# Performance work log

Measured on AMD Instinct MI355X. Metric: run time of the kernel, lower is better.

Reference implementation:

```python
import jax, jax.numpy as jnp
import numpy as np

B, T, N, C = 4, 2048, 4, 1024   # batch, seq, expansion_rate, hidden_dim
A = 8                            # max_lora_adapters
SINKHORN_ITERS = 20
EPS = 1e-05


def _logit(x):
    x = jnp.clip(x, 1e-06, 1.0 - 1e-06)
    return jnp.log(x) - jnp.log(1.0 - x)


def setup_inputs() -> dict:
    key = jax.random.key(0)
    ks = jax.random.split(key, 12)
    nC = N * C
    x = jax.random.normal(ks[0], (B, T, N, C), dtype=jnp.float32)
    adapter_indices = jax.random.randint(ks[1], (B,), 0, A)
    # Learned parameters (perturbed from the identity init so gradients are non-trivial)
    input_norm_weight = 1.0 + 0.02 * jax.random.normal(ks[2], (A, nC), dtype=jnp.float32)
    phi_pre = 0.02 * jax.random.normal(ks[3], (A, nC, N), dtype=jnp.float32)
    phi_post = 0.02 * jax.random.normal(ks[4], (A, nC, N), dtype=jnp.float32)
    phi_res = 0.02 * jax.random.normal(ks[5], (A, nC, N * N), dtype=jnp.float32)
    b_pre = _logit(jnp.float32(1.0 / N)) + 0.1 * jax.random.normal(ks[6], (A, N), dtype=jnp.float32)
    b_post = 0.1 * jax.random.normal(ks[7], (A, N), dtype=jnp.float32)
    b_res = 10.0 * jnp.eye(N, dtype=jnp.float32) + jax.random.normal(ks[8], (A, N, N), dtype=jnp.float32)
    alpha_pre = 1.0 + 0.1 * jax.random.normal(ks[9], (A,), dtype=jnp.float32)
    alpha_post = 1.0 + 0.1 * jax.random.normal(ks[10], (A,), dtype=jnp.float32)
    alpha_res = 1.0 + 0.1 * jax.random.normal(ks[11], (A,), dtype=jnp.float32)
    return {
        "x": x,
        "input_norm_weight": input_norm_weight,
        "phi_pre": phi_pre, "phi_post": phi_post, "phi_res": phi_res,
        "b_pre": b_pre, "b_post": b_post, "b_res": b_res,
        "alpha_pre": alpha_pre, "alpha_post": alpha_post, "alpha_res": alpha_res,
        "adapter_indices": adapter_indices,
    }


def _sinkhorn_knopp(M, iters):
    M = jnp.exp(M)
    def step(_, mat):
        mat = mat / mat.sum(axis=-1, keepdims=True)
        mat = mat / mat.sum(axis=-2, keepdims=True)
        return mat
    return jax.lax.fori_loop(0, iters, step, M)


def reference(x, input_norm_weight, phi_pre, phi_post, phi_res,
              b_pre, b_post, b_res, alpha_pre, alpha_post, alpha_res,
              adapter_indices):
    Bb, Tt, n, Cc = x.shape
    idx = adapter_indices.astype(jnp.int32)
    x_flat = x.reshape(Bb, Tt, n * Cc)
    # adapter-indexed RMSNorm
    w = input_norm_weight[idx]                                  # [B, nC]
    rms = jnp.sqrt(jnp.mean(x_flat ** 2, axis=-1, keepdims=True) + EPS)
    x_norm = w[:, None, :] * x_flat / rms                       # [B, T, nC]
    # pre: input-dependent aggregation weights H_pre
    pre_logits = jnp.einsum('btd,bdn->btn', x_norm, phi_pre[idx])
    H_pre = jax.nn.sigmoid(alpha_pre[idx][:, None, None] * pre_logits + b_pre[idx][:, None, :])
    x_agg = (H_pre[..., None] * x).sum(axis=-2)                 # [B, T, C]
    output = x_agg                                              # identity block between pre and post
    # post: distribution weights H_post and doubly-stochastic mixing M
    post_logits = jnp.einsum('btd,bdn->btn', x_norm, phi_post[idx])
    H_post = 2.0 * jax.nn.sigmoid(alpha_post[idx][:, None, None] * post_logits + b_post[idx][:, None, :])
    res_logits = jnp.einsum('btd,bdm->btm', x_norm, phi_res[idx]).reshape(Bb, Tt, n, n)
    tilde_H_res = alpha_res[idx][:, None, None, None] * res_logits + b_res[idx][:, None, :, :]
    M = _sinkhorn_knopp(tilde_H_res, SINKHORN_ITERS)            # [B, T, n, n]
    y_dist = H_post[..., None] * output[..., None, :]           # [B, T, n, C]
    x_mixed = jnp.einsum('btij,btjc->btic', M, x)               # [B, T, n, C]
    return x_mixed + y_dist
```

## Files before the change

### kernel.cpp

```cpp
#include <hip/hip_runtime.h>


#define BT 8192
#define NC 4096
#define NC4 1024

__global__ __launch_bounds__(256, 3) void lora_connector_kernel(
    const float* __restrict__ x,
    const float* __restrict__ inw,
    const float* __restrict__ phi_pre,
    const float* __restrict__ phi_post,
    const float* __restrict__ phi_res,
    const float* __restrict__ b_pre,
    const float* __restrict__ b_post,
    const float* __restrict__ b_res,
    const float* __restrict__ alpha_pre,
    const float* __restrict__ alpha_post,
    const float* __restrict__ alpha_res,
    const int*   __restrict__ adapter_indices,
    float* __restrict__ out)
{
    const int tid = threadIdx.x;
    const int g   = tid & 3;
    const int l   = tid >> 2;
    const int wvid= tid >> 6;
    const int ln  = tid & 63;
    const int blk = blockIdx.x;
    const int b   = blk >> 9;
    const int idx = adapter_indices[b];

    const float4* __restrict__ pp4 = (const float4*)(phi_pre  + (size_t)idx * (NC * 4));
    const float4* __restrict__ po4 = (const float4*)(phi_post + (size_t)idx * (NC * 4));
    const float4* __restrict__ pr4 = (const float4*)(phi_res  + (size_t)idx * (NC * 16));
    const float*  __restrict__ inwp = inw + (size_t)idx * NC + tid;
    const float*  __restrict__ xb   = x + (size_t)(blk * 4) * NC + tid;

    __shared__ float4 tileL[2][1536];
    __shared__ float red[4][4][26];

    const float4* sg[6];
    int sstr[6];
    #pragma unroll
    for (int i = 0; i < 6; ++i) {
        const int c = wvid * 6 + i;
        const float4* bp; int off, str;
        if (c < 8) {
            bp  = (c < 4) ? pp4 : po4;
            off = ((c & 3) << 6) + ln;
            str = 256;
        } else {
            const int k = c - 8;
            bp  = pr4;
            off = ((((k & 3) << 6) + ln) << 2) + (k >> 2);
            str = 1024;
        }
        sg[i] = bp + off;
        sstr[i] = str;
    }

    #define STAGE_TILE(MT, BF)                                                   \
    {                                                                            \
        _Pragma("unroll")                                                        \
        for (int i = 0; i < 6; ++i) {                                            \
            __builtin_amdgcn_global_load_lds(                                    \
                (const __attribute__((address_space(1))) void*)(sg[i] + (size_t)(MT) * sstr[i]), \
                (__attribute__((address_space(3))) void*)&tileL[BF][(wvid * 6 + i) << 6], \
                16, 0, 0);                                                       \
        }                                                                        \
    }

    STAGE_TILE(0, 0);

    float acc[24][4];
    float ss[4];
    #pragma unroll
    for (int j = 0; j < 24; ++j) {
        acc[j][0] = 0.0f; acc[j][1] = 0.0f; acc[j][2] = 0.0f; acc[j][3] = 0.0f;
    }
    ss[0] = ss[1] = ss[2] = ss[3] = 0.0f;

    float xn[4], wn;
    #pragma unroll
    for (int j = 0; j < 4; ++j) xn[j] = xb[j * NC];
    wn = inwp[0];

    #pragma unroll 1
    for (int m = 0; m < 16; ++m) {
        const int bf = m & 1;
        __syncthreads();
        if (m < 15) STAGE_TILE(m + 1, bf ^ 1);

        const float wv = wn;
        float s[4];
        #pragma unroll
        for (int j = 0; j < 4; ++j) {
            const float xv = xn[j];
            s[j] = xv * wv;
            ss[j] = fmaf(xv, xv, ss[j]);
        }
        if (m < 15) {
            #pragma unroll
            for (int j = 0; j < 4; ++j) xn[j] = xb[j * NC + (m + 1) * 256];
            wn = inwp[(m + 1) * 256];
        }

        const float4 a = tileL[bf][tid];
        #pragma unroll
        for (int j = 0; j < 4; ++j) {
            acc[0][j] = fmaf(s[j], a.x, acc[0][j]);
            acc[1][j] = fmaf(s[j], a.y, acc[1][j]);
            acc[2][j] = fmaf(s[j], a.z, acc[2][j]);
            acc[3][j] = fmaf(s[j], a.w, acc[3][j]);
        }
        const float4 p = tileL[bf][256 + tid];
        #pragma unroll
        for (int j = 0; j < 4; ++j) {
            acc[4][j] = fmaf(s[j], p.x, acc[4][j]);
            acc[5][j] = fmaf(s[j], p.y, acc[5][j]);
            acc[6][j] = fmaf(s[j], p.z, acc[6][j]);
            acc[7][j] = fmaf(s[j], p.w, acc[7][j]);
        }
        #pragma unroll
        for (int q = 0; q < 4; ++q) {
            const float4 r = tileL[bf][512 + q * 256 + tid];
            #pragma unroll
            for (int j = 0; j < 4; ++j) {
                acc[8 + q * 4 + 0][j] = fmaf(s[j], r.x, acc[8 + q * 4 + 0][j]);
                acc[8 + q * 4 + 1][j] = fmaf(s[j], r.y, acc[8 + q * 4 + 1][j]);
                acc[8 + q * 4 + 2][j] = fmaf(s[j], r.z, acc[8 + q * 4 + 2][j]);
                acc[8 + q * 4 + 3][j] = fmaf(s[j], r.w, acc[8 + q * 4 + 3][j]);
            }
        }
    }

    float tot[25];
    #define RED4(V0, V1, V2, V3, DST)                                   \
    {                                                                   \
        const float u0 = (V0) + __shfl_xor((V0), 1);                    \
        const float u1 = (V1) + __shfl_xor((V1), 1);                    \
        const float u2 = (V2) + __shfl_xor((V2), 1);                    \
        const float u3 = (V3) + __shfl_xor((V3), 1);                    \
        const float r0 = (ln & 1) ? u1 : u0;                            \
        const float r1 = (ln & 1) ? u3 : u2;                            \
        const float w0 = r0 + __shfl_xor(r0, 2);                        \
        const float w1 = r1 + __shfl_xor(r1, 2);                        \
        float tv = (ln & 2) ? w1 : w0;                                  \
        tv += __shfl_xor(tv, 4);  tv += __shfl_xor(tv, 8);              \
        tv += __shfl_xor(tv, 16); tv += __shfl_xor(tv, 32);             \
        (DST) = tv;                                                     \
    }
    #pragma unroll
    for (int j = 0; j < 24; ++j)
        RED4(acc[j][0], acc[j][1], acc[j][2], acc[j][3], tot[j]);
    RED4(ss[0], ss[1], ss[2], ss[3], tot[24]);
    #undef RED4

    if (ln < 4) {
        #pragma unroll
        for (int j = 0; j < 25; ++j) red[wvid][ln][j] = tot[j];
    }
    __syncthreads();
    #pragma unroll
    for (int j = 0; j < 25; ++j)
        tot[j] = (red[0][g][j] + red[1][g][j]) + (red[2][g][j] + red[3][g][j]);

    const float inv_rms = rsqrtf(tot[24] * (1.0f / 4096.0f) + 1e-5f);
    const float apre  = alpha_pre[idx];
    const float apost = alpha_post[idx];
    const float ares  = alpha_res[idx];

    float Hpre[4], Hpost[4];
    #pragma unroll
    for (int n = 0; n < 4; ++n) {
        const float zp = fmaf(apre,  tot[n]     * inv_rms, b_pre[idx * 4 + n]);
        Hpre[n]  = 1.0f / (1.0f + __expf(-zp));
        const float zq = fmaf(apost, tot[4 + n] * inv_rms, b_post[idx * 4 + n]);
        Hpost[n] = 2.0f / (1.0f + __expf(-zq));
    }

    const int s16 = ln >> 2;
    const int sj = s16 & 3;
    const int si = s16 >> 2;
    float Mv = __expf(fmaf(ares, tot[8 + si * 4 + sj] * inv_rms,
                           b_res[idx * 16 + si * 4 + sj]));
    #pragma unroll
    for (int it = 0; it < 20; ++it) {
        float rs = Mv + __shfl_xor(Mv, 4);
        rs += __shfl_xor(rs, 8);
        Mv *= __builtin_amdgcn_rcpf(rs);
        float cs = Mv + __shfl_xor(Mv, 16);
        cs += __shfl_xor(cs, 32);
        Mv *= __builtin_amdgcn_rcpf(cs);
    }

    float W[4][4];
    #pragma unroll
    for (int sq = 0; sq < 16; ++sq) {
        const float mm = __shfl(Mv, sq * 4 + g);
        W[sq >> 2][sq & 3] = fmaf(Hpost[sq >> 2], Hpre[sq & 3], mm);
    }

    const int tok = blk * 4 + g;
    const float4* __restrict__ x4p = (const float4*)x + (size_t)tok * NC4;
    float4* __restrict__ out4 = (float4*)out + (size_t)tok * NC4;
    #pragma unroll
    for (int k = 0; k < 4; ++k) {
        const int c4 = k * 64 + l;
        const float4 x0 = x4p[0 * 256 + c4];
        const float4 x1 = x4p[1 * 256 + c4];
        const float4 x2 = x4p[2 * 256 + c4];
        const float4 x3 = x4p[3 * 256 + c4];
        #pragma unroll
        for (int i = 0; i < 4; ++i) {
            float4 o;
            o.x = fmaf(W[i][0], x0.x, fmaf(W[i][1], x1.x, fmaf(W[i][2], x2.x, W[i][3] * x3.x)));
            o.y = fmaf(W[i][0], x0.y, fmaf(W[i][1], x1.y, fmaf(W[i][2], x2.y, W[i][3] * x3.y)));
            o.z = fmaf(W[i][0], x0.z, fmaf(W[i][1], x1.z, fmaf(W[i][2], x2.z, W[i][3] * x3.z)));
            o.w = fmaf(W[i][0], x0.w, fmaf(W[i][1], x1.w, fmaf(W[i][2], x2.w, W[i][3] * x3.w)));
            out4[i * 256 + c4] = o;
        }
    }
    #undef STAGE_TILE
}

extern "C" void kernel_launch(void* const* d_in, const int* in_sizes, int n_in,
                              void* d_out, int out_size, void* d_ws, size_t ws_size,
                              hipStream_t stream) {
    const float* x         = (const float*)d_in[0];
    const float* inw       = (const float*)d_in[1];
    const float* phi_pre   = (const float*)d_in[2];
    const float* phi_post  = (const float*)d_in[3];
    const float* phi_res   = (const float*)d_in[4];
    const float* b_pre     = (const float*)d_in[5];
    const float* b_post    = (const float*)d_in[6];
    const float* b_res     = (const float*)d_in[7];
    const float* alpha_pre = (const float*)d_in[8];
    const float* alpha_post= (const float*)d_in[9];
    const float* alpha_res = (const float*)d_in[10];
    const int*   adapter   = (const int*)d_in[11];
    float* out = (float*)d_out;

    dim3 grid(BT / 4);
    dim3 block(256);
    lora_connector_kernel<<<grid, block, 0, stream>>>(
        x, inw, phi_pre, phi_post, phi_res,
        b_pre, b_post, b_res,
        alpha_pre, alpha_post, alpha_res,
        adapter, out);
}
```

Before: 333.0 us.

## Split projection outputs across block halves to halve accumulator registers

Each half of the 256-thread block now accumulates 12 of the 24 projection outputs over 128-element d-tiles, with twice as many tiles (32 instead of 16). The half-size LDS double buffer and the 48 accumulators per thread instead of 96 aim to relieve register pressure and raise occupancy, which is why the minimum-blocks launch bound is dropped. In exchange, both halves load the same x and norm-weight values, there are more loop iterations and barriers, and the cross-wave reduction is remapped. The LDS destination address passed to global_load_lds now includes a per-lane offset, which may not match how that builtin addresses LDS.

```diff
diff --git a/kernel.cpp b/kernel.cpp
--- a/kernel.cpp
+++ b/kernel.cpp
@@ -4,8 +4,10 @@
 #define BT 8192
 #define NC 4096
 #define NC4 1024
-
-__global__ __launch_bounds__(256, 3) void lora_connector_kernel(
+#define NT 32
+#define TD 128
+
+__global__ __launch_bounds__(256) void lora_connector_kernel(
     const float* __restrict__ x,
     const float* __restrict__ inw,
     const float* __restrict__ phi_pre,
@@ -25,6 +27,8 @@
     const int l   = tid >> 2;
     const int wvid= tid >> 6;
     const int ln  = tid & 63;
+    const int dl  = tid & 127;
+    const int half= tid >> 7;
     const int blk = blockIdx.x;
     const int b   = blk >> 9;
     const int idx = adapter_indices[b];
@@ -32,27 +36,27 @@
     const float4* __restrict__ pp4 = (const float4*)(phi_pre  + (size_t)idx * (NC * 4));
     const float4* __restrict__ po4 = (const float4*)(phi_post + (size_t)idx * (NC * 4));
     const float4* __restrict__ pr4 = (const float4*)(phi_res  + (size_t)idx * (NC * 16));
-    const float*  __restrict__ inwp = inw + (size_t)idx * NC + tid;
-    const float*  __restrict__ xb   = x + (size_t)(blk * 4) * NC + tid;
-
-    __shared__ float4 tileL[2][1536];
-    __shared__ float red[4][4][26];
-
-    const float4* sg[6];
-    int sstr[6];
-    #pragma unroll
-    for (int i = 0; i < 6; ++i) {
-        const int c = wvid * 6 + i;
+    const float*  __restrict__ inwp = inw + (size_t)idx * NC + dl;
+    const float*  __restrict__ xb   = x + (size_t)(blk * 4) * NC + dl;
+
+    __shared__ float4 tileL[2][768];
+    __shared__ float red[4][4][14];
+
+    const float4* sg[3];
+    int sstr[3];
+    #pragma unroll
+    for (int i = 0; i < 3; ++i) {
+        const int c = wvid * 3 + i;
         const float4* bp; int off, str;
-        if (c < 8) {
-            bp  = (c < 4) ? pp4 : po4;
-            off = ((c & 3) << 6) + ln;
-            str = 256;
+        if (c < 4) {
+            bp  = (c < 2) ? pp4 : po4;
+            off = ((c & 1) << 6) + ln;
+            str = TD;
         } else {
-            const int k = c - 8;
+            const int k = c - 4;
             bp  = pr4;
-            off = ((((k & 3) << 6) + ln) << 2) + (k >> 2);
-            str = 1024;
+            off = ((((k & 1) << 6) + ln) << 2) + (k >> 1);
+            str = TD * 4;
         }
         sg[i] = bp + off;
         sstr[i] = str;
@@ -61,20 +65,20 @@
     #define STAGE_TILE(MT, BF)                                                   \
     {                                                                            \
         _Pragma("unroll")                                                        \
-        for (int i = 0; i < 6; ++i) {                                            \
+        for (int i = 0; i < 3; ++i) {                                            \
             __builtin_amdgcn_global_load_lds(                                    \
                 (const __attribute__((address_space(1))) void*)(sg[i] + (size_t)(MT) * sstr[i]), \
-                (__attribute__((address_space(3))) void*)&tileL[BF][(wvid * 6 + i) << 6], \
+                (__attribute__((address_space(3))) void*)&tileL[BF][((wvid * 3 + i) << 6) + ln], \
                 16, 0, 0);                                                       \
         }                                                                        \
     }
 
     STAGE_TILE(0, 0);
 
-    float acc[24][4];
+    float acc[12][4];
     float ss[4];
     #pragma unroll
-    for (int j = 0; j < 24; ++j) {
+    for (int j = 0; j < 12; ++j) {
         acc[j][0] = 0.0f; acc[j][1] = 0.0f; acc[j][2] = 0.0f; acc[j][3] = 0.0f;
     }
     ss[0] = ss[1] = ss[2] = ss[3] = 0.0f;
@@ -84,11 +88,13 @@
     for (int j = 0; j < 4; ++j) xn[j] = xb[j * NC];
     wn = inwp[0];
 
+    const int ba = half * 384 + dl;
+
     #pragma unroll 1
-    for (int m = 0; m < 16; ++m) {
+    for (int m = 0; m < NT; ++m) {
         const int bf = m & 1;
         __syncthreads();
-        if (m < 15) STAGE_TILE(m + 1, bf ^ 1);
+        if (m < NT - 1) STAGE_TILE(m + 1, bf ^ 1);
 
         const float wv = wn;
         float s[4];
@@ -98,42 +104,33 @@
             s[j] = xv * wv;
             ss[j] = fmaf(xv, xv, ss[j]);
         }
-        if (m < 15) {
+        if (m < NT - 1) {
             #pragma unroll
-            for (int j = 0; j < 4; ++j) xn[j] = xb[j * NC + (m + 1) * 256];
-            wn = inwp[(m + 1) * 256];
-        }
-
-        const float4 a = tileL[bf][tid];
+            for (int j = 0; j < 4; ++j) xn[j] = xb[j * NC + (m + 1) * TD];
+            wn = inwp[(m + 1) * TD];
+        }
+
+        const float4 a = tileL[bf][ba];
+        const float4 p = tileL[bf][ba + 128];
+        const float4 r = tileL[bf][ba + 256];
         #pragma unroll
         for (int j = 0; j < 4; ++j) {
-            acc[0][j] = fmaf(s[j], a.x, acc[0][j]);
-            acc[1][j] = fmaf(s[j], a.y, acc[1][j]);
-            acc[2][j] = fmaf(s[j], a.z, acc[2][j]);
-            acc[3][j] = fmaf(s[j], a.w, acc[3][j]);
-        }
-        const float4 p = tileL[bf][256 + tid];
-        #pragma unroll
-        for (int j = 0; j < 4; ++j) {
-            acc[4][j] = fmaf(s[j], p.x, acc[4][j]);
-            acc[5][j] = fmaf(s[j], p.y, acc[5][j]);
-            acc[6][j] = fmaf(s[j], p.z, acc[6][j]);
-            acc[7][j] = fmaf(s[j], p.w, acc[7][j]);
-        }
-        #pragma unroll
-        for (int q = 0; q < 4; ++q) {
-            const float4 r = tileL[bf][512 + q * 256 + tid];
-            #pragma unroll
-            for (int j = 0; j < 4; ++j) {
-                acc[8 + q * 4 + 0][j] = fmaf(s[j], r.x, acc[8 + q * 4 + 0][j]);
-                acc[8 + q * 4 + 1][j] = fmaf(s[j], r.y, acc[8 + q * 4 + 1][j]);
-                acc[8 + q * 4 + 2][j] = fmaf(s[j], r.z, acc[8 + q * 4 + 2][j]);
-                acc[8 + q * 4 + 3][j] = fmaf(s[j], r.w, acc[8 + q * 4 + 3][j]);
-            }
-        }
-    }
-
-    float tot[25];
+            acc[0][j]  = fmaf(s[j], a.x, acc[0][j]);
+            acc[1][j]  = fmaf(s[j], a.y, acc[1][j]);
+            acc[2][j]  = fmaf(s[j], a.z, acc[2][j]);
+            acc[3][j]  = fmaf(s[j], a.w, acc[3][j]);
+            acc[4][j]  = fmaf(s[j], p.x, acc[4][j]);
+            acc[5][j]  = fmaf(s[j], p.y, acc[5][j]);
+            acc[6][j]  = fmaf(s[j], p.z, acc[6][j]);
+            acc[7][j]  = fmaf(s[j], p.w, acc[7][j]);
+            acc[8][j]  = fmaf(s[j], r.x, acc[8][j]);
+            acc[9][j]  = fmaf(s[j], r.y, acc[9][j]);
+            acc[10][j] = fmaf(s[j], r.z, acc[10][j]);
+            acc[11][j] = fmaf(s[j], r.w, acc[11][j]);
+        }
+    }
+
+    float t12[13];
     #define RED4(V0, V1, V2, V3, DST)                                   \
     {                                                                   \
         const float u0 = (V0) + __shfl_xor((V0), 1);                    \
@@ -150,19 +147,23 @@
         (DST) = tv;                                                     \
     }
     #pragma unroll
-    for (int j = 0; j < 24; ++j)
-        RED4(acc[j][0], acc[j][1], acc[j][2], acc[j][3], tot[j]);
-    RED4(ss[0], ss[1], ss[2], ss[3], tot[24]);
+    for (int j = 0; j < 12; ++j)
+        RED4(acc[j][0], acc[j][1], acc[j][2], acc[j][3], t12[j]);
+    RED4(ss[0], ss[1], ss[2], ss[3], t12[12]);
     #undef RED4
 
     if (ln < 4) {
         #pragma unroll
-        for (int j = 0; j < 25; ++j) red[wvid][ln][j] = tot[j];
+        for (int j = 0; j < 13; ++j) red[wvid][ln][j] = t12[j];
     }
     __syncthreads();
-    #pragma unroll
-    for (int j = 0; j < 25; ++j)
-        tot[j] = (red[0][g][j] + red[1][g][j]) + (red[2][g][j] + red[3][g][j]);
+    float tot[25];
+    #pragma unroll
+    for (int j = 0; j < 12; ++j) {
+        tot[j]      = red[0][g][j] + red[1][g][j];
+        tot[12 + j] = red[2][g][j] + red[3][g][j];
+    }
+    tot[24] = red[0][g][12] + red[1][g][12];
 
     const float inv_rms = rsqrtf(tot[24] * (1.0f / 4096.0f) + 1e-5f);
     const float apre  = alpha_pre[idx];
```

Result: faster. 309.8 us (-6.9%).
